# Optimization experiments

Measured on AMD Instinct MI355X. Metric: run time of the kernel, lower is better.

Reference implementation:

```python
import jax, jax.numpy as jnp
import numpy as np

D_MODEL = 1024
N_HEADS = 16
D_K = D_MODEL // N_HEADS
ROPE_THETA = 10000.0
SOFT_CAP = 50.0  # Gemma-2-style logit soft cap
B, S = 4, 2048


def _rope(x, pos, theta=ROPE_THETA):
    # x: [..., S, d_k], interleaved-pair rotation
    d_k = x.shape[-1]
    inv_freq = theta ** (-jnp.arange(0, d_k, 2, dtype=jnp.float32) / d_k)  # [d_k/2]
    ang = pos.astype(jnp.float32)[:, None] * inv_freq[None, :]             # [S, d_k/2]
    cos, sin = jnp.cos(ang), jnp.sin(ang)
    x1, x2 = x[..., 0::2], x[..., 1::2]
    out_even = x1 * cos - x2 * sin
    out_odd = x1 * sin + x2 * cos
    return jnp.stack([out_even, out_odd], axis=-1).reshape(x.shape)


def setup_inputs() -> dict:
    key = jax.random.key(0)
    kx, kqkv, kout = jax.random.split(key, 3)
    scale = D_MODEL ** -0.5
    x = jax.random.normal(kx, (B, S, D_MODEL), dtype=jnp.float32)
    w_qkv = jax.random.normal(kqkv, (3 * D_MODEL, D_MODEL), dtype=jnp.float32) * scale
    w_out = jax.random.normal(kout, (D_MODEL, D_MODEL), dtype=jnp.float32) * scale
    return {"x": x, "w_qkv": w_qkv, "w_out": w_out}


def reference(x, w_qkv, w_out):
    b, s, d = x.shape
    # fused QKV projection (Linear, no bias): [B,S,3D]
    qkv = jnp.einsum('bsd,ed->bse', x, w_qkv)
    # '(n h d_k)' split -> [3, B, H, S, d_k]
    qkv = qkv.reshape(b, s, 3, N_HEADS, D_K)
    qkv = jnp.transpose(qkv, (2, 0, 3, 1, 4))
    q, k, v = qkv[0], qkv[1], qkv[2]
    pos = jnp.arange(s)
    q = _rope(q, pos)
    k = _rope(k, pos)
    scores = jnp.einsum('bhqd,bhkd->bhqk', q, k) / jnp.float32(D_K) ** 0.5
    scores = SOFT_CAP * jnp.tanh(scores / SOFT_CAP)  # cap_logits
    causal = jnp.tril(jnp.ones((s, s), dtype=bool))
    scores = jnp.where(causal, scores, jnp.float32(-1e30))
    attn = jax.nn.softmax(scores, axis=-1)
    out = jnp.einsum('bhqk,bhkd->bhqd', attn, v)
    out = jnp.transpose(out, (0, 2, 1, 3)).reshape(b, s, d)  # (h d_v) merge
    return jnp.einsum('bsd,ed->bse', out, w_out)
```

## Files before the change

### kernel.cpp

```cpp
#include <hip/hip_runtime.h>
#include <stdint.h>

#define S_LEN 2048
#define NH    16
#define DK    64
#define DM    1024

typedef __attribute__((ext_vector_type(8))) __bf16 bf16x8;
typedef __attribute__((ext_vector_type(8))) unsigned short u16x8;
typedef __attribute__((ext_vector_type(4))) float  f32x4;

static __device__ __forceinline__ unsigned short f2bf(float f) {
    union { float f; unsigned int u; } v; v.f = f;
    unsigned int r = v.u + 0x7FFFu + ((v.u >> 16) & 1u);
    return (unsigned short)(r >> 16);
}

static __device__ __forceinline__ float cap_exp2(float sp) {
    float u = exp2f(sp);
    float w = __builtin_amdgcn_rcpf(u + 1.0f);
    return exp2f(__builtin_fmaf(w, -144.2695040888f, 72.1347520444f));
}

#define GLL(src_, dst_) __builtin_amdgcn_global_load_lds(                              \
    (const __attribute__((address_space(1))) unsigned int*)(src_),                     \
    (__attribute__((address_space(3))) unsigned int*)(dst_), 16, 0, 0)

__global__ void detect_f32(const unsigned short* __restrict__ x, int* __restrict__ flag)
{
    __shared__ int tot;
    if (threadIdx.x == 0) tot = 0;
    __syncthreads();
    int weird = 0;
    for (int i = threadIdx.x; i < 16384; i += 256) {
        int e = (x[i] >> 7) & 0xFF;
        if (e == 0 || e < 87 || e > 167) weird++;
    }
    atomicAdd(&tot, weird);
    __syncthreads();
    if (threadIdx.x == 0) *flag = (tot > 4000) ? 1 : 0;
}

__global__ __launch_bounds__(256) void norm_bf16(const void* __restrict__ src,
                                                 unsigned short* __restrict__ dst,
                                                 int n, const int* __restrict__ flag)
{
    const int isf32 = *flag;
    int i = (blockIdx.x * 256 + threadIdx.x) * 8;
    if (i >= n) return;
    if (isf32) {
        const float* p = (const float*)src + i;
        u16x8 o;
        o[0] = f2bf(p[0]); o[1] = f2bf(p[1]); o[2] = f2bf(p[2]); o[3] = f2bf(p[3]);
        o[4] = f2bf(p[4]); o[5] = f2bf(p[5]); o[6] = f2bf(p[6]); o[7] = f2bf(p[7]);
        *(u16x8*)&dst[i] = o;
    } else {
        *(uint4*)&dst[i] = *(const uint4*)((const unsigned short*)src + i);
    }
}

__global__ __launch_bounds__(256) void rope_tab(float2* __restrict__ tab)
{
    int e = blockIdx.x * 256 + threadIdx.x;
    int s = e >> 5, d2 = e & 31;
    float invf = exp2f(-(float)d2 * 0.41524101186f);
    float sn, cs;
    sincosf((float)s * invf, &sn, &cs);
    tab[e] = make_float2(cs, sn);
}

#define VST  136

#define MFMA(a, b, c) __builtin_amdgcn_mfma_f32_16x16x32_bf16((a), (b), (c), 0, 0, 0)

#define GEMM_MAIN(Aptr, Wptr, lda_, ldw_)                                              \
    f32x4 zz = {0.f, 0.f, 0.f, 0.f};                                                   \
    f32x4 c00=zz,c01=zz,c02=zz,c03=zz, c10=zz,c11=zz,c12=zz,c13=zz,                    \
          c20=zz,c21=zz,c22=zz,c23=zz, c30=zz,c31=zz,c32=zz,c33=zz;                    \
    const int strow_ = wave * 16 + (lane >> 2);                                        \
    const int sgr_   = (((lane & 3) ^ ((strow_ >> 1) & 3))) << 3;                      \
    const unsigned short* Ag_ = (Aptr) + (size_t)(m0 + strow_) * (lda_) + sgr_;        \
    const unsigned short* Bg_ = (Wptr) + (size_t)(n0 + strow_) * (ldw_) + sgr_;        \
    const int kfG_ = ((quad ^ ((l16 >> 1) & 3))) << 3;                                 \
    {                                                                                  \
        unsigned short* Ad_ = As + wave * 512;                                         \
        unsigned short* Bd_ = Bs + wave * 512;                                         \
        GLL(Ag_, Ad_); GLL(Ag_ + 64 * (size_t)(lda_), Ad_ + 2048);                     \
        GLL(Bg_, Bd_); GLL(Bg_ + 64 * (size_t)(ldw_), Bd_ + 2048);                     \
    }                                                                                  \
    __syncthreads();                                  \
    int cbuf_ = 0;                                                                     \
    for (int k0 = 0; k0 < 1024; k0 += 32) {                                            \
        if (k0 + 32 < 1024) {                                                          \
            unsigned short* Ad_ = As + ((cbuf_ ^ 1) << 12) + wave * 512;               \
            unsigned short* Bd_ = Bs + ((cbuf_ ^ 1) << 12) + wave * 512;               \
            GLL(Ag_ + k0 + 32, Ad_);                                                   \
            GLL(Ag_ + k0 + 32 + 64 * (size_t)(lda_), Ad_ + 2048);                      \
            GLL(Bg_ + k0 + 32, Bd_);                                                   \
            GLL(Bg_ + k0 + 32 + 64 * (size_t)(ldw_), Bd_ + 2048);                      \
        }                                                                              \
        const unsigned short* Ar_ = As + (cbuf_ << 12);                                \
        const unsigned short* Br_ = Bs + (cbuf_ << 12);                                \
        bf16x8 a0 = *(const bf16x8*)&Ar_[(wm +  0 + l16) * 32 + kfG_];                 \
        bf16x8 a1 = *(const bf16x8*)&Ar_[(wm + 16 + l16) * 32 + kfG_];                 \
        bf16x8 a2 = *(const bf16x8*)&Ar_[(wm + 32 + l16) * 32 + kfG_];                 \
        bf16x8 a3 = *(const bf16x8*)&Ar_[(wm + 48 + l16) * 32 + kfG_];                 \
        bf16x8 b0 = *(const bf16x8*)&Br_[(wn +  0 + l16) * 32 + kfG_];                 \
        bf16x8 b1 = *(const bf16x8*)&Br_[(wn + 16 + l16) * 32 + kfG_];                 \
        bf16x8 b2 = *(const bf16x8*)&Br_[(wn + 32 + l16) * 32 + kfG_];                 \
        bf16x8 b3 = *(const bf16x8*)&Br_[(wn + 48 + l16) * 32 + kfG_];                 \
        c00 = MFMA(a0, b0, c00); c01 = MFMA(a0, b1, c01);                              \
        c02 = MFMA(a0, b2, c02); c03 = MFMA(a0, b3, c03);                              \
        c10 = MFMA(a1, b0, c10); c11 = MFMA(a1, b1, c11);                              \
        c12 = MFMA(a1, b2, c12); c13 = MFMA(a1, b3, c13);                              \
        c20 = MFMA(a2, b0, c20); c21 = MFMA(a2, b1, c21);                              \
        c22 = MFMA(a2, b2, c22); c23 = MFMA(a2, b3, c23);                              \
        c30 = MFMA(a3, b0, c30); c31 = MFMA(a3, b1, c31);                              \
        c32 = MFMA(a3, b2, c32); c33 = MFMA(a3, b3, c33);                              \
        __syncthreads();                    \
        cbuf_ ^= 1;                                                                    \
    }

__global__ __launch_bounds__(256) void gemm_fused(const unsigned short* __restrict__ A,
                                                  const unsigned short* __restrict__ W,
                                                  const float2* __restrict__ tab,
                                                  unsigned short* __restrict__ qr,
                                                  unsigned short* __restrict__ kr,
                                                  unsigned short* __restrict__ vt)
{
    __shared__ __align__(16) unsigned short smem[128 * VST];
    unsigned short* As = smem;
    unsigned short* Bs = smem + 8192;

    const int tid  = threadIdx.x;
    const int wave = tid >> 6;
    const int lane = tid & 63;
    const int quad = lane >> 4;
    const int l16  = lane & 15;
    const int m0 = blockIdx.y * 128;
    const int n0 = blockIdx.x * 128;
    const int wm = (wave >> 1) * 64;
    const int wn = (wave & 1) * 64;

    GEMM_MAIN(A, W, 1024, 1024)

    const int cls = n0 >> 10;
    if (cls < 2) {
        unsigned short* dst = cls ? kr : qr;
        const float qs = cls ? 1.0f : 0.125f * 0.0577078016f;

#define ROPE_R(accv, MTc, rc, even_, h_, d_) do {                                      \
        int row = m0 + wm + (MTc) * 16 + quad * 4 + (rc);                              \
        int s = row & (S_LEN - 1), b = row >> 11;                                      \
        float2 cssn = tab[(s << 5) + ((d_) >> 1)];                                     \
        float own = accv[rc];                                                          \
        float oth = __shfl_xor(own, 1);                                                \
        float res = (even_) ? (own * cssn.x - oth * cssn.y)                            \
                            : (oth * cssn.y + own * cssn.x);                           \
        dst[((size_t)(b * NH + (h_)) * S_LEN + s) * DK + (d_)] = f2bf(res * qs);       \
    } while (0)

#define ROPE_ST(accv, MTc, NTc) do {                                                   \
        int col = (n0 & 1023) + wn + (NTc) * 16 + l16;                                 \
        int h = col >> 6, d = col & 63;                                                \
        int even = !(d & 1);                                                           \
        ROPE_R(accv, MTc, 0, even, h, d);                                              \
        ROPE_R(accv, MTc, 1, even, h, d);                                              \
        ROPE_R(accv, MTc, 2, even, h, d);                                              \
        ROPE_R(accv, MTc, 3, even, h, d);                                              \
    } while (0)

        ROPE_ST(c00, 0, 0); ROPE_ST(c01, 0, 1); ROPE_ST(c02, 0, 2); ROPE_ST(c03, 0, 3);
        ROPE_ST(c10, 1, 0); ROPE_ST(c11, 1, 1); ROPE_ST(c12, 1, 2); ROPE_ST(c13, 1, 3);
        ROPE_ST(c20, 2, 0); ROPE_ST(c21, 2, 1); ROPE_ST(c22, 2, 2); ROPE_ST(c23, 2, 3);
        ROPE_ST(c30, 3, 0); ROPE_ST(c31, 3, 1); ROPE_ST(c32, 3, 2); ROPE_ST(c33, 3, 3);
    } else {
        __syncthreads();

#define VST_ACC(accv, MTc, NTc) do {                                                   \
        int dl = wn + (NTc) * 16 + l16;                                                \
        int base = dl * VST + wm + (MTc) * 16 + quad * 4;                              \
        smem[base + 0] = f2bf(accv[0]); smem[base + 1] = f2bf(accv[1]);                \
        smem[base + 2] = f2bf(accv[2]); smem[base + 3] = f2bf(accv[3]);                \
    } while (0)

        VST_ACC(c00, 0, 0); VST_ACC(c01, 0, 1); VST_ACC(c02, 0, 2); VST_ACC(c03, 0, 3);
        VST_ACC(c10, 1, 0); VST_ACC(c11, 1, 1); VST_ACC(c12, 1, 2); VST_ACC(c13, 1, 3);
        VST_ACC(c20, 2, 0); VST_ACC(c21, 2, 1); VST_ACC(c22, 2, 2); VST_ACC(c23, 2, 3);
        VST_ACC(c30, 3, 0); VST_ACC(c31, 3, 1); VST_ACC(c32, 3, 2); VST_ACC(c33, 3, 3);
        __syncthreads();
        int dl = tid >> 1, sh = (tid & 1) * 64;
        int vcol = (n0 - 2048) + dl;
        int h = vcol >> 6, dd = vcol & 63;
        int b = m0 >> 11, s0 = m0 & (S_LEN - 1);
        unsigned short* dst = vt + (((size_t)(b * NH + h) * DK + dd) * S_LEN + s0 + sh);
        const unsigned short* src = smem + dl * VST + sh;
#pragma unroll
        for (int i = 0; i < 64; i += 8)
            *(bf16x8*)&dst[i] = *(const bf16x8*)&src[i];
    }
}

__global__ __launch_bounds__(256) void gemm_out(const unsigned short* __restrict__ A,
                                                const unsigned short* __restrict__ W,
                                                float* __restrict__ C)
{
    __shared__ __align__(16) unsigned short As[8192];
    __shared__ __align__(16) unsigned short Bs[8192];
    const int tid  = threadIdx.x;
    const int wave = tid >> 6;
    const int lane = tid & 63;
    const int quad = lane >> 4;
    const int l16  = lane & 15;
    const int m0 = blockIdx.y * 128;
    const int n0 = blockIdx.x * 128;
    const int wm = (wave >> 1) * 64;
    const int wn = (wave & 1) * 64;

    GEMM_MAIN(A, W, 1024, 1024)

#define OUT_ST(accv, MTc, NTc) do {                                                    \
    int col = n0 + wn + (NTc) * 16 + l16;                                              \
    int rowb = m0 + wm + (MTc) * 16 + quad * 4;                                        \
    C[(size_t)(rowb + 0) * 1024 + col] = accv[0];                                      \
    C[(size_t)(rowb + 1) * 1024 + col] = accv[1];                                      \
    C[(size_t)(rowb + 2) * 1024 + col] = accv[2];                                      \
    C[(size_t)(rowb + 3) * 1024 + col] = accv[3];                                      \
} while (0)

    OUT_ST(c00, 0, 0); OUT_ST(c01, 0, 1); OUT_ST(c02, 0, 2); OUT_ST(c03, 0, 3);
    OUT_ST(c10, 1, 0); OUT_ST(c11, 1, 1); OUT_ST(c12, 1, 2); OUT_ST(c13, 1, 3);
    OUT_ST(c20, 2, 0); OUT_ST(c21, 2, 1); OUT_ST(c22, 2, 2); OUT_ST(c23, 2, 3);
    OUT_ST(c30, 3, 0); OUT_ST(c31, 3, 1); OUT_ST(c32, 3, 2); OUT_ST(c33, 3, 3);
}

__global__ __launch_bounds__(256) void attn_fwd(const unsigned short* __restrict__ qr,
                                                const unsigned short* __restrict__ kr,
                                                const unsigned short* __restrict__ vt,
                                                unsigned short* __restrict__ aout)
{
    __shared__ __align__(16) unsigned short kvs[2][2][4096];
    __shared__ __align__(16) unsigned short plds[4][1024];
    int blk  = blockIdx.x;
    int pr   = blk & 15;
    int bh   = blk >> 4;
    int b    = bh >> 4, h = bh & 15;
    int wave = threadIdx.x >> 6;
    int lane = threadIdx.x & 63;
    int quad = lane >> 4, l16 = lane & 15;

    const unsigned short* kbase = kr + (size_t)bh * S_LEN * DK;
    const unsigned short* vbase = vt + (size_t)bh * DK * S_LEN;
    unsigned short* pw = &plds[wave][0];

    u16x8 onesu = {0x3F80,0x3F80,0x3F80,0x3F80,0x3F80,0x3F80,0x3F80,0x3F80};
    bf16x8 vones = *(bf16x8*)&onesu;

    const int lam3  = lane >> 3;
    const int sc3p  = (lane & 7) ^ lam3;
    const int strow = wave * 8 + lam3;
    const int stcol = sc3p * 8;
    const int kfA = l16 * 64 + ((quad ^ (l16 & 7)) << 3);

#define STAGE(c_, nb_) do {                                                            \
    const int j0s = (c_) * 64;                                                         \
    unsigned short* kd = &kvs[nb_][0][wave * 512];                                     \
    unsigned short* vd = &kvs[nb_][1][wave * 512];                                     \
    const unsigned short* kg = kbase + (size_t)(j0s + strow) * 64 + stcol;             \
    const unsigned short* vg = vbase + (size_t)strow * S_LEN + j0s + stcol;            \
    GLL(kg, kd); GLL(kg + 32 * 64, kd + 2048);                                         \
    GLL(vg, vd); GLL(vg + 32 * S_LEN, vd + 2048);                                      \
} while (0)

#define QK_LDS(kb_) do {                                                               \
    bf16x8 ka, kb;                                                                     \
    ka = *(const bf16x8*)&(kb_)[kfA];          kb = *(const bf16x8*)&(kb_)[kfA ^ 32];  \
    sc0 = MFMA(qf0, ka, sc0); sc0 = MFMA(qf1, kb, sc0);                                \
    ka = *(const bf16x8*)&(kb_)[kfA + 1024];   kb = *(const bf16x8*)&(kb_)[(kfA + 1024) ^ 32]; \
    sc1 = MFMA(qf0, ka, sc1); sc1 = MFMA(qf1, kb, sc1);                                \
    ka = *(const bf16x8*)&(kb_)[kfA + 2048];   kb = *(const bf16x8*)&(kb_)[(kfA + 2048) ^ 32]; \
    sc2 = MFMA(qf0, ka, sc2); sc2 = MFMA(qf1, kb, sc2);                                \
    ka = *(const bf16x8*)&(kb_)[kfA + 3072];   kb = *(const bf16x8*)&(kb_)[(kfA + 3072) ^ 32]; \
    sc3 = MFMA(qf0, ka, sc3); sc3 = MFMA(qf1, kb, sc3);                                \
} while (0)

#define PV_LDS(vb_) do {                                                               \
    bf16x8 pf0 = *(const bf16x8*)&pw[kfA];                                             \
    bf16x8 pf1 = *(const bf16x8*)&pw[kfA ^ 32];                                        \
    bf16x8 va, vb;                                                                     \
    va = *(const bf16x8*)&(vb_)[kfA];          vb = *(const bf16x8*)&(vb_)[kfA ^ 32];  \
    o0 = MFMA(pf0, va, o0); o0 = MFMA(pf1, vb, o0);                                    \
    va = *(const bf16x8*)&(vb_)[kfA + 1024];   vb = *(const bf16x8*)&(vb_)[(kfA + 1024) ^ 32]; \
    o1 = MFMA(pf0, va, o1); o1 = MFMA(pf1, vb, o1);                                    \
    va = *(const bf16x8*)&(vb_)[kfA + 2048];   vb = *(const bf16x8*)&(vb_)[(kfA + 2048) ^ 32]; \
    o2 = MFMA(pf0, va, o2); o2 = MFMA(pf1, vb, o2);                                    \
    va = *(const bf16x8*)&(vb_)[kfA + 3072];   vb = *(const bf16x8*)&(vb_)[(kfA + 3072) ^ 32]; \
    o3 = MFMA(pf0, va, o3); o3 = MFMA(pf1, vb, o3);                                    \
    o4 = MFMA(pf0, vones, o4); o4 = MFMA(pf1, vones, o4);                              \
} while (0)

#define P_STORE(rc, p0_, p1_, p2_, p3_) do {                                           \
    unsigned int r01, r23;                                                             \
    asm("v_cvt_pk_bf16_f32 %0, %1, %2" : "=v"(r01) : "v"(p0_), "v"(p1_));              \
    asm("v_cvt_pk_bf16_f32 %0, %1, %2" : "=v"(r23) : "v"(p2_), "v"(p3_));              \
    const int row_ = quad * 4 + (rc);                                                  \
    const int r7_  = row_ & 7;                                                         \
    const int pb_  = row_ * 64 + (l16 & 7);                                            \
    const int lh_  = l16 >> 3;                                                         \
    pw[pb_ + ((( lh_     ^ r7_) << 3))] = (unsigned short)r01;                         \
    pw[pb_ + (((2 | lh_) ^ r7_) << 3)]  = (unsigned short)(r01 >> 16);                 \
    pw[pb_ + (((4 | lh_) ^ r7_) << 3)]  = (unsigned short)r23;                         \
    pw[pb_ + (((6 | lh_) ^ r7_) << 3)]  = (unsigned short)(r23 >> 16);                 \
} while (0)

#define ROW_UPD_N(rc) do {                                                             \
    float p0 = cap_exp2(sc0[rc]);                                                      \
    float p1 = cap_exp2(sc1[rc]);                                                      \
    float p2 = cap_exp2(sc2[rc]);                                                      \
    float p3 = cap_exp2(sc3[rc]);                                                      \
    P_STORE(rc, p0, p1, p2, p3);                                                       \
} while (0)

#define ROW_UPD_M(rc) do {                                                             \
    int qrow = q0w + quad * 4 + (rc);                                                  \
    float p0 = (j0 + l16      > qrow) ? 0.f : cap_exp2(sc0[rc]);                       \
    float p1 = (j0 + 16 + l16 > qrow) ? 0.f : cap_exp2(sc1[rc]);                       \
    float p2 = (j0 + 32 + l16 > qrow) ? 0.f : cap_exp2(sc2[rc]);                       \
    float p3 = (j0 + 48 + l16 > qrow) ? 0.f : cap_exp2(sc3[rc]);                       \
    P_STORE(rc, p0, p1, p2, p3);                                                       \
} while (0)

    for (int side = 0; side < 2; ++side) {
        const int qblk = side ? (31 - pr) : pr;
        const int q0w  = qblk * 64 + wave * 16;

        const unsigned short* qbase = qr + ((size_t)bh * S_LEN + q0w) * DK;
        bf16x8 qf0 = *(const bf16x8*)&qbase[l16 * DK + quad * 8];
        bf16x8 qf1 = *(const bf16x8*)&qbase[l16 * DK + 32 + quad * 8];

        f32x4 zz = {0.f, 0.f, 0.f, 0.f};
        f32x4 o0 = zz, o1 = zz, o2 = zz, o3 = zz, o4 = zz;

        const int nch = qblk + 1;

        STAGE(0, 0);
        asm volatile("s_waitcnt vmcnt(0)" ::: "memory");
        __syncthreads();
        int cb = 0;

        for (int c = 0; c < nch - 1; ++c) {
            STAGE(c + 1, cb ^ 1);
            f32x4 sc0 = zz, sc1 = zz, sc2 = zz, sc3 = zz;
            QK_LDS(&kvs[cb][0][0]);
            ROW_UPD_N(0); ROW_UPD_N(1); ROW_UPD_N(2); ROW_UPD_N(3);
            asm volatile("s_waitcnt lgkmcnt(0)" ::: "memory");
            PV_LDS(&kvs[cb][1][0]);
            asm volatile("s_waitcnt vmcnt(0)" ::: "memory");
            __syncthreads();
            cb ^= 1;
        }

        {
            const int j0 = (nch - 1) * 64;
            f32x4 sc0 = zz, sc1 = zz, sc2 = zz, sc3 = zz;
            QK_LDS(&kvs[cb][0][0]);
            ROW_UPD_M(0); ROW_UPD_M(1); ROW_UPD_M(2); ROW_UPD_M(3);
            asm volatile("s_waitcnt lgkmcnt(0)" ::: "memory");
            PV_LDS(&kvs[cb][1][0]);
            __syncthreads();
        }

#define OUT_ROW(rc) do {                                                               \
        int qrow = q0w + quad * 4 + (rc);                                              \
        size_t off = (size_t)(b * S_LEN + qrow) * DM + h * DK + l16;                   \
        float rl = 1.0f / o4[rc];                                                      \
        aout[off +  0] = f2bf(o0[rc] * rl);                                            \
        aout[off + 16] = f2bf(o1[rc] * rl);                                            \
        aout[off + 32] = f2bf(o2[rc] * rl);                                            \
        aout[off + 48] = f2bf(o3[rc] * rl);                                            \
} while (0)

        OUT_ROW(0); OUT_ROW(1); OUT_ROW(2); OUT_ROW(3);
#undef OUT_ROW
    }
}

extern "C" void kernel_launch(void* const* d_in, const int* in_sizes, int n_in,
                              void* d_out, int out_size, void* d_ws, size_t ws_size,
                              hipStream_t stream)
{
    const void* x = nullptr; const void* wqkv = nullptr; const void* wout = nullptr;
    for (int i = 0; i < n_in; ++i) {
        if      (in_sizes[i] == 8388608) x    = d_in[i];
        else if (in_sizes[i] == 3145728) wqkv = d_in[i];
        else if (in_sizes[i] == 1048576) wout = d_in[i];
    }
    float* out = (float*)d_out;
    unsigned short* ws   = (unsigned short*)d_ws;
    unsigned short* ob16 = (unsigned short*)d_out;

    unsigned short* qr     = ws;
    unsigned short* kr     = ws + (size_t)8388608;
    unsigned short* aout   = ws + (size_t)16777216;
    int* flag              = (int*)(ws + (size_t)25165824);
    unsigned short* wqkvbf = aout;
    unsigned short* woutbf = qr;
    float2* tab            = (float2*)(ws + (size_t)16777216 + 4194304);

    unsigned short* vt  = ob16;
    unsigned short* xbf = ob16 + (size_t)8388608;

    detect_f32<<<1, 256, 0, stream>>>((const unsigned short*)x, flag);
    norm_bf16<<<4096, 256, 0, stream>>>(x, xbf, 8388608, flag);
    norm_bf16<<<1536, 256, 0, stream>>>(wqkv, wqkvbf, 3145728, flag);
    rope_tab<<<256, 256, 0, stream>>>(tab);
    gemm_fused<<<dim3(24, 64), 256, 0, stream>>>(xbf, wqkvbf, tab, qr, kr, vt);
    attn_fwd<<<1024, 256, 0, stream>>>(qr, kr, vt, aout);
    norm_bf16<<<512, 256, 0, stream>>>(wout, woutbf, 1048576, flag);
    gemm_out<<<dim3(8, 64), 256, 0, stream>>>(aout, woutbf, out);
}
```

Baseline: 313.1 us.

## Share K/V tiles across paired query blocks and merge prep kernels

The attention kernel used to process its two paired query blocks one after the other, loading K/V tiles twice. It now processes both in a single loop over the longer causal range, so each staged K/V tile feeds both query blocks. The three preprocessing kernels are merged into one launch, and the bf16 copy is skipped when inputs are already bf16 by letting the GEMMs pick the source pointer from a flag. The trade-off is more live registers for the second set of accumulators and Q fragments, which may lower occupancy.

After: 320.2 us. +2.3%, slower.

```diff
diff --git a/kernel.cpp b/kernel.cpp
--- a/kernel.cpp
+++ b/kernel.cpp
@@ -41,32 +41,45 @@
     if (threadIdx.x == 0) *flag = (tot > 4000) ? 1 : 0;
 }
 
-__global__ __launch_bounds__(256) void norm_bf16(const void* __restrict__ src,
+__global__ __launch_bounds__(256) void prep(const void* __restrict__ x,
+                                            const void* __restrict__ wqkv,
+                                            unsigned short* __restrict__ xbf,
+                                            unsigned short* __restrict__ wqkvbf,
+                                            float2* __restrict__ tab,
+                                            const int* __restrict__ flag)
+{
+    int bid = blockIdx.x;
+    if (bid < 256) {
+        int e = bid * 256 + threadIdx.x;
+        int s = e >> 5, d2 = e & 31;
+        float invf = exp2f(-(float)d2 * 0.41524101186f);
+        float sn, cs;
+        sincosf((float)s * invf, &sn, &cs);
+        tab[e] = make_float2(cs, sn);
+        return;
+    }
+    if (!*flag) return;
+    const float* src; unsigned short* dst; int i;
+    if (bid < 4352) { src = (const float*)x;    dst = xbf;    i = ((bid - 256)  * 256 + threadIdx.x) * 8; }
+    else            { src = (const float*)wqkv; dst = wqkvbf; i = ((bid - 4352) * 256 + threadIdx.x) * 8; }
+    const float* p = src + i;
+    u16x8 o;
+    o[0] = f2bf(p[0]); o[1] = f2bf(p[1]); o[2] = f2bf(p[2]); o[3] = f2bf(p[3]);
+    o[4] = f2bf(p[4]); o[5] = f2bf(p[5]); o[6] = f2bf(p[6]); o[7] = f2bf(p[7]);
+    *(u16x8*)&dst[i] = o;
+}
+
+__global__ __launch_bounds__(256) void norm_wout(const void* __restrict__ src,
                                                  unsigned short* __restrict__ dst,
-                                                 int n, const int* __restrict__ flag)
-{
-    const int isf32 = *flag;
+                                                 const int* __restrict__ flag)
+{
+    if (!*flag) return;
     int i = (blockIdx.x * 256 + threadIdx.x) * 8;
-    if (i >= n) return;
-    if (isf32) {
-        const float* p = (const float*)src + i;
-        u16x8 o;
-        o[0] = f2bf(p[0]); o[1] = f2bf(p[1]); o[2] = f2bf(p[2]); o[3] = f2bf(p[3]);
-        o[4] = f2bf(p[4]); o[5] = f2bf(p[5]); o[6] = f2bf(p[6]); o[7] = f2bf(p[7]);
-        *(u16x8*)&dst[i] = o;
-    } else {
-        *(uint4*)&dst[i] = *(const uint4*)((const unsigned short*)src + i);
-    }
-}
-
-__global__ __launch_bounds__(256) void rope_tab(float2* __restrict__ tab)
-{
-    int e = blockIdx.x * 256 + threadIdx.x;
-    int s = e >> 5, d2 = e & 31;
-    float invf = exp2f(-(float)d2 * 0.41524101186f);
-    float sn, cs;
-    sincosf((float)s * invf, &sn, &cs);
-    tab[e] = make_float2(cs, sn);
+    const float* p = (const float*)src + i;
+    u16x8 o;
+    o[0] = f2bf(p[0]); o[1] = f2bf(p[1]); o[2] = f2bf(p[2]); o[3] = f2bf(p[3]);
+    o[4] = f2bf(p[4]); o[5] = f2bf(p[5]); o[6] = f2bf(p[6]); o[7] = f2bf(p[7]);
+    *(u16x8*)&dst[i] = o;
 }
 
 #define VST  136
@@ -121,8 +134,11 @@
         cbuf_ ^= 1;                                                                    \
     }
 
-__global__ __launch_bounds__(256) void gemm_fused(const unsigned short* __restrict__ A,
-                                                  const unsigned short* __restrict__ W,
+__global__ __launch_bounds__(256) void gemm_fused(const unsigned short* __restrict__ x0,
+                                                  const unsigned short* __restrict__ xc,
+                                                  const unsigned short* __restrict__ w0,
+                                                  const unsigned short* __restrict__ wc,
+                                                  const int* __restrict__ flag,
                                                   const float2* __restrict__ tab,
                                                   unsigned short* __restrict__ qr,
                                                   unsigned short* __restrict__ kr,
@@ -131,6 +147,10 @@
     __shared__ __align__(16) unsigned short smem[128 * VST];
     unsigned short* As = smem;
     unsigned short* Bs = smem + 8192;
+
+    const int isf32 = *flag;
+    const unsigned short* A = isf32 ? xc : x0;
+    const unsigned short* W = isf32 ? wc : w0;
 
     const int tid  = threadIdx.x;
     const int wave = tid >> 6;
@@ -202,11 +222,14 @@
 }
 
 __global__ __launch_bounds__(256) void gemm_out(const unsigned short* __restrict__ A,
-                                                const unsigned short* __restrict__ W,
+                                                const unsigned short* __restrict__ w0,
+                                                const unsigned short* __restrict__ wc,
+                                                const int* __restrict__ flag,
                                                 float* __restrict__ C)
 {
     __shared__ __align__(16) unsigned short As[8192];
     __shared__ __align__(16) unsigned short Bs[8192];
+    const unsigned short* W = *flag ? wc : w0;
     const int tid  = threadIdx.x;
     const int wave = tid >> 6;
     const int lane = tid & 63;
@@ -272,31 +295,31 @@
     GLL(vg, vd); GLL(vg + 32 * S_LEN, vd + 2048);                                      \
 } while (0)
 
-#define QK_LDS(kb_) do {                                                               \
+#define QK_LDS(kb_, qf0_, qf1_) do {                                                   \
     bf16x8 ka, kb;                                                                     \
     ka = *(const bf16x8*)&(kb_)[kfA];          kb = *(const bf16x8*)&(kb_)[kfA ^ 32];  \
-    sc0 = MFMA(qf0, ka, sc0); sc0 = MFMA(qf1, kb, sc0);                                \
+    sc0 = MFMA(qf0_, ka, sc0); sc0 = MFMA(qf1_, kb, sc0);                              \
     ka = *(const bf16x8*)&(kb_)[kfA + 1024];   kb = *(const bf16x8*)&(kb_)[(kfA + 1024) ^ 32]; \
-    sc1 = MFMA(qf0, ka, sc1); sc1 = MFMA(qf1, kb, sc1);                                \
+    sc1 = MFMA(qf0_, ka, sc1); sc1 = MFMA(qf1_, kb, sc1);                              \
     ka = *(const bf16x8*)&(kb_)[kfA + 2048];   kb = *(const bf16x8*)&(kb_)[(kfA + 2048) ^ 32]; \
-    sc2 = MFMA(qf0, ka, sc2); sc2 = MFMA(qf1, kb, sc2);                                \
+    sc2 = MFMA(qf0_, ka, sc2); sc2 = MFMA(qf1_, kb, sc2);                              \
     ka = *(const bf16x8*)&(kb_)[kfA + 3072];   kb = *(const bf16x8*)&(kb_)[(kfA + 3072) ^ 32]; \
-    sc3 = MFMA(qf0, ka, sc3); sc3 = MFMA(qf1, kb, sc3);                                \
-} while (0)
-
-#define PV_LDS(vb_) do {                                                               \
+    sc3 = MFMA(qf0_, ka, sc3); sc3 = MFMA(qf1_, kb, sc3);                              \
+} while (0)
+
+#define PV_LDS(vb_, o0_, o1_, o2_, o3_, o4_) do {                                      \
     bf16x8 pf0 = *(const bf16x8*)&pw[kfA];                                             \
     bf16x8 pf1 = *(const bf16x8*)&pw[kfA ^ 32];                                        \
     bf16x8 va, vb;                                                                     \
     va = *(const bf16x8*)&(vb_)[kfA];          vb = *(const bf16x8*)&(vb_)[kfA ^ 32];  \
-    o0 = MFMA(pf0, va, o0); o0 = MFMA(pf1, vb, o0);                                    \
+    o0_ = MFMA(pf0, va, o0_); o0_ = MFMA(pf1, vb, o0_);                                \
     va = *(const bf16x8*)&(vb_)[kfA + 1024];   vb = *(const bf16x8*)&(vb_)[(kfA + 1024) ^ 32]; \
-    o1 = MFMA(pf0, va, o1); o1 = MFMA(pf1, vb, o1);                                    \
+    o1_ = MFMA(pf0, va, o1_); o1_ = MFMA(pf1, vb, o1_);                                \
     va = *(const bf16x8*)&(vb_)[kfA + 2048];   vb = *(const bf16x8*)&(vb_)[(kfA + 2048) ^ 32]; \
-    o2 = MFMA(pf0, va, o2); o2 = MFMA(pf1, vb, o2);                                    \
+    o2_ = MFMA(pf0, va, o2_); o2_ = MFMA(pf1, vb, o2_);                                \
     va = *(const bf16x8*)&(vb_)[kfA + 3072];   vb = *(const bf16x8*)&(vb_)[(kfA + 3072) ^ 32]; \
-    o3 = MFMA(pf0, va, o3); o3 = MFMA(pf1, vb, o3);                                    \
-    o4 = MFMA(pf0, vones, o4); o4 = MFMA(pf1, vones, o4);                              \
+    o3_ = MFMA(pf0, va, o3_); o3_ = MFMA(pf1, vb, o3_);                                \
+    o4_ = MFMA(pf0, vones, o4_); o4_ = MFMA(pf1, vones, o4_);                          \
 } while (0)
 
 #define P_STORE(rc, p0_, p1_, p2_, p3_) do {                                           \
@@ -321,8 +344,8 @@
     P_STORE(rc, p0, p1, p2, p3);                                                       \
 } while (0)
 
-#define ROW_UPD_M(rc) do {                                                             \
-    int qrow = q0w + quad * 4 + (rc);                                                  \
+#define ROW_UPD_M(rc, q0w_) do {                                                       \
+    int qrow = (q0w_) + quad * 4 + (rc);                                               \
     float p0 = (j0 + l16      > qrow) ? 0.f : cap_exp2(sc0[rc]);                       \
     float p1 = (j0 + 16 + l16 > qrow) ? 0.f : cap_exp2(sc1[rc]);                       \
     float p2 = (j0 + 32 + l16 > qrow) ? 0.f : cap_exp2(sc2[rc]);                       \
@@ -330,59 +353,77 @@
     P_STORE(rc, p0, p1, p2, p3);                                                       \
 } while (0)
 
-    for (int side = 0; side < 2; ++side) {
-        const int qblk = side ? (31 - pr) : pr;
-        const int q0w  = qblk * 64 + wave * 16;
-
-        const unsigned short* qbase = qr + ((size_t)bh * S_LEN + q0w) * DK;
-        bf16x8 qf0 = *(const bf16x8*)&qbase[l16 * DK + quad * 8];
-        bf16x8 qf1 = *(const bf16x8*)&qbase[l16 * DK + 32 + quad * 8];
-
-        f32x4 zz = {0.f, 0.f, 0.f, 0.f};
-        f32x4 o0 = zz, o1 = zz, o2 = zz, o3 = zz, o4 = zz;
-
-        const int nch = qblk + 1;
-
-        STAGE(0, 0);
+    const int nchA = pr + 1;
+    const int nchB = 32 - pr;
+    const int q0wA = pr * 64 + wave * 16;
+    const int q0wB = (31 - pr) * 64 + wave * 16;
+
+    const unsigned short* qbA = qr + ((size_t)bh * S_LEN + q0wA) * DK;
+    const unsigned short* qbB = qr + ((size_t)bh * S_LEN + q0wB) * DK;
+    bf16x8 qfA0 = *(const bf16x8*)&qbA[l16 * DK + quad * 8];
+    bf16x8 qfA1 = *(const bf16x8*)&qbA[l16 * DK + 32 + quad * 8];
+    bf16x8 qfB0 = *(const bf16x8*)&qbB[l16 * DK + quad * 8];
+    bf16x8 qfB1 = *(const bf16x8*)&qbB[l16 * DK + 32 + quad * 8];
+
+    f32x4 zz = {0.f, 0.f, 0.f, 0.f};
+    f32x4 oA0 = zz, oA1 = zz, oA2 = zz, oA3 = zz, oA4 = zz;
+    f32x4 oB0 = zz, oB1 = zz, oB2 = zz, oB3 = zz, oB4 = zz;
+
+    STAGE(0, 0);
+    asm volatile("s_waitcnt vmcnt(0)" ::: "memory");
+    __syncthreads();
+    int cb = 0;
+
+    for (int c = 0; c < nchB; ++c) {
+        const int j0 = c * 64;
+        if (c + 1 < nchB) STAGE(c + 1, cb ^ 1);
+
+        {
+            f32x4 sc0 = zz, sc1 = zz, sc2 = zz, sc3 = zz;
+            QK_LDS(&kvs[cb][0][0], qfB0, qfB1);
+            if (c == nchB - 1) { ROW_UPD_M(0, q0wB); ROW_UPD_M(1, q0wB);
+                                 ROW_UPD_M(2, q0wB); ROW_UPD_M(3, q0wB); }
+            else               { ROW_UPD_N(0); ROW_UPD_N(1);
+                                 ROW_UPD_N(2); ROW_UPD_N(3); }
+            asm volatile("s_waitcnt lgkmcnt(0)" ::: "memory");
+            PV_LDS(&kvs[cb][1][0], oB0, oB1, oB2, oB3, oB4);
+        }
+
+        if (c < nchA) {
+            f32x4 sc0 = zz, sc1 = zz, sc2 = zz, sc3 = zz;
+            QK_LDS(&kvs[cb][0][0], qfA0, qfA1);
+            if (c == nchA - 1) { ROW_UPD_M(0, q0wA); ROW_UPD_M(1, q0wA);
+                                 ROW_UPD_M(2, q0wA); ROW_UPD_M(3, q0wA); }
+            else               { ROW_UPD_N(0); ROW_UPD_N(1);
+                                 ROW_UPD_N(2); ROW_UPD_N(3); }
+            asm volatile("s_waitcnt lgkmcnt(0)" ::: "memory");
+            PV_LDS(&kvs[cb][1][0], oA0, oA1, oA2, oA3, oA4);
+        }
+
         asm volatile("s_waitcnt vmcnt(0)" ::: "memory");
         __syncthreads();
-        int cb = 0;
-
-        for (int c = 0; c < nch - 1; ++c) {
-            STAGE(c + 1, cb ^ 1);
-            f32x4 sc0 = zz, sc1 = zz, sc2 = zz, sc3 = zz;
-            QK_LDS(&kvs[cb][0][0]);
-            ROW_UPD_N(0); ROW_UPD_N(1); ROW_UPD_N(2); ROW_UPD_N(3);
-            asm volatile("s_waitcnt lgkmcnt(0)" ::: "memory");
-            PV_LDS(&kvs[cb][1][0]);
-            asm volatile("s_waitcnt vmcnt(0)" ::: "memory");
-            __syncthreads();
-            cb ^= 1;
-        }
-
-        {
-            const int j0 = (nch - 1) * 64;
-            f32x4 sc0 = zz, sc1 = zz, sc2 = zz, sc3 = zz;
-            QK_LDS(&kvs[cb][0][0]);
-            ROW_UPD_M(0); ROW_UPD_M(1); ROW_UPD_M(2); ROW_UPD_M(3);
-            asm volatile("s_waitcnt lgkmcnt(0)" ::: "memory");
-            PV_LDS(&kvs[cb][1][0]);
-            __syncthreads();
-        }
-
-#define OUT_ROW(rc) do {                                                               \
-        int qrow = q0w + quad * 4 + (rc);                                              \
-        size_t off = (size_t)(b * S_LEN + qrow) * DM + h * DK + l16;                   \
-        float rl = 1.0f / o4[rc];                                                      \
-        aout[off +  0] = f2bf(o0[rc] * rl);                                            \
-        aout[off + 16] = f2bf(o1[rc] * rl);                                            \
-        aout[off + 32] = f2bf(o2[rc] * rl);                                            \
-        aout[off + 48] = f2bf(o3[rc] * rl);                                            \
-} while (0)
-
-        OUT_ROW(0); OUT_ROW(1); OUT_ROW(2); OUT_ROW(3);
+        cb ^= 1;
+    }
+
+#define OUT_ROW(rc, q0w_, a0_, a1_, a2_, a3_, a4_) do {                                \
+    int qrow = (q0w_) + quad * 4 + (rc);                                               \
+    size_t off = (size_t)(b * S_LEN + qrow) * DM + h * DK + l16;                       \
+    float rl = 1.0f / a4_[rc];                                                         \
+    aout[off +  0] = f2bf(a0_[rc] * rl);                                               \
+    aout[off + 16] = f2bf(a1_[rc] * rl);                                               \
+    aout[off + 32] = f2bf(a2_[rc] * rl);                                               \
+    aout[off + 48] = f2bf(a3_[rc] * rl);                                               \
+} while (0)
+
+    OUT_ROW(0, q0wA, oA0, oA1, oA2, oA3, oA4);
+    OUT_ROW(1, q0wA, oA0, oA1, oA2, oA3, oA4);
+    OUT_ROW(2, q0wA, oA0, oA1, oA2, oA3, oA4);
+    OUT_ROW(3, q0wA, oA0, oA1, oA2, oA3, oA4);
+    OUT_ROW(0, q0wB, oB0, oB1, oB2, oB3, oB4);
+    OUT_ROW(1, q0wB, oB0, oB1, oB2, oB3, oB4);
+    OUT_ROW(2, q0wB, oB0, oB1, oB2, oB3, oB4);
+    OUT_ROW(3, q0wB, oB0, oB1, oB2, oB3, oB4);
 #undef OUT_ROW
-    }
 }
 
 extern "C" void kernel_launch(void* const* d_in, const int* in_sizes, int n_in,
@@ -411,11 +452,13 @@
     unsigned short* xbf = ob16 + (size_t)8388608;
 
     detect_f32<<<1, 256, 0, stream>>>((const unsigned short*)x, flag);
-    norm_bf16<<<4096, 256, 0, stream>>>(x, xbf, 8388608, flag);
-    norm_bf16<<<1536, 256, 0, stream>>>(wqkv, wqkvbf, 3145728, flag);
-    rope_tab<<<256, 256, 0, stream>>>(tab);
-    gemm_fused<<<dim3(24, 64), 256, 0, stream>>>(xbf, wqkvbf, tab, qr, kr, vt);
+    prep<<<5888, 256, 0, stream>>>(x, wqkv, xbf, wqkvbf, tab, flag);
+    gemm_fused<<<dim3(24, 64), 256, 0, stream>>>((const unsigned short*)x, xbf,
+                                                 (const unsigned short*)wqkv, wqkvbf,
+                                                 flag, tab, qr, kr, vt);
     attn_fwd<<<1024, 256, 0, stream>>>(qr, kr, vt, aout);
-    norm_bf16<<<512, 256, 0, stream>>>(wout, woutbf, 1048576, flag);
-    gemm_out<<<dim3(8, 64), 256, 0, stream>>>(aout, woutbf, out);
-}
+    norm_wout<<<512, 256, 0, stream>>>(wout, woutbf, flag);
+    gemm_out<<<dim3(8, 64), 256, 0, stream>>>(aout,
+                                              (const unsigned short*)wout, woutbf,
+                                              flag, out);
+}
```
